# Kernel tuning notes

Hardware: AMD Instinct MI355X
Metric: run time of the kernel (lower is better)

## Reference

```python
import jax, jax.numpy as jnp
import numpy as np

D_MODEL = 1024
NUM_HEADS = 16
B, S = 2, 2048


def setup_inputs() -> dict:
    key = jax.random.key(0)
    ks = jax.random.split(key, 11)
    scale = 1.0 / np.sqrt(D_MODEL)
    inp = {
        'q': jax.random.normal(ks[0], (B, S, D_MODEL), jnp.float32),
        'k': jax.random.normal(ks[1], (B, S, D_MODEL), jnp.float32),
        'v': jax.random.normal(ks[2], (B, S, D_MODEL), jnp.float32),
        'w_q': jax.random.normal(ks[3], (D_MODEL, D_MODEL), jnp.float32) * scale,
        'b_q': jax.random.normal(ks[4], (D_MODEL,), jnp.float32) * 0.01,
        'w_k': jax.random.normal(ks[5], (D_MODEL, D_MODEL), jnp.float32) * scale,
        'b_k': jax.random.normal(ks[6], (D_MODEL,), jnp.float32) * 0.01,
        'w_v': jax.random.normal(ks[7], (D_MODEL, D_MODEL), jnp.float32) * scale,
        'b_v': jax.random.normal(ks[8], (D_MODEL,), jnp.float32) * 0.01,
        'w_o': jax.random.normal(ks[9], (D_MODEL, D_MODEL), jnp.float32) * scale,
        'b_o': jax.random.normal(ks[10], (D_MODEL,), jnp.float32) * 0.01,
    }
    return inp


def reference(q, k, v, w_q, b_q, w_k, b_k, w_v, b_v, w_o, b_o):
    Bq, Sq, D = q.shape
    H = NUM_HEADS
    dh = D // H
    # projections (weights stored as [in, out])
    query = q @ w_q + b_q
    key = k @ w_k + b_k
    value = v @ w_v + b_v
    # [B, S, D] -> [B, H, S, dh]
    query = query.reshape(Bq, Sq, H, dh).transpose(0, 2, 1, 3)
    key = key.reshape(Bq, -1, H, dh).transpose(0, 2, 1, 3)
    value = value.reshape(Bq, -1, H, dh).transpose(0, 2, 1, 3)
    # NOTE: original module does NOT scale by 1/sqrt(dh)
    scores = jnp.einsum('bhqd,bhkd->bhqk', query, key)  # [B,H,S,S]
    causal_mask = jnp.triu(jnp.ones((Sq, Sq), dtype=bool), k=1)  # True above diag
    scores = jnp.where(causal_mask[None, None], -jnp.inf, scores)
    attn = jax.nn.softmax(scores, axis=-1)
    data = jnp.einsum('bhqk,bhkd->bhqd', attn, value)  # [B,H,S,dh]
    # FAITHFUL to original bug: transpose(0,1) then view(B, S, -1)
    data = data.transpose(1, 0, 2, 3).reshape(Bq, Sq, -1)  # [H,B,S,dh] -> [B,S,D]
    return data @ w_o + b_o
```

## Files before the change

### kernel.cpp

```cpp
#include <hip/hip_runtime.h>

typedef __fp16 f16;
typedef __fp16 f16x8 __attribute__((ext_vector_type(8)));
typedef __fp16 f16x4 __attribute__((ext_vector_type(4)));
typedef __fp16 f16x2 __attribute__((ext_vector_type(2)));
typedef float f32x4 __attribute__((ext_vector_type(4)));
typedef float f32x16 __attribute__((ext_vector_type(16)));

#define D_MODEL 1024
#define SEQ 2048
#define NH 16
#define MTOT 4096

typedef const __attribute__((address_space(1))) unsigned int* gp1_t;
typedef __attribute__((address_space(3))) unsigned int* lp3_t;

__device__ __forceinline__ void gload_lds16(const void* g, void* l) {
  __builtin_amdgcn_global_load_lds((gp1_t)g, (lp3_t)l, 16, 0, 0);
}

__device__ __forceinline__ int permrow(int r) {
  int bp = r >> 11, u = (r >> 7) & 15, t = r & 127;
  int g16 = (bp << 4) | u;
  return ((((g16 & 1) << 4) | (g16 >> 1)) << 7) + t;
}

__device__ __forceinline__ unsigned int pkrtz(float a, float b) {
  union { f16x2 h; unsigned int u; } z;
  z.h = __builtin_amdgcn_cvt_pkrtz(a, b);
  return z.u;
}

__global__ __launch_bounds__(256) void cvt_all(const float* __restrict__ q,
                                               const float* __restrict__ k,
                                               const float* __restrict__ v,
                                               const float* __restrict__ wq,
                                               const float* __restrict__ wk,
                                               const float* __restrict__ wv,
                                               const float* __restrict__ wo,
                                               f16* __restrict__ qkv16,
                                               f16* __restrict__ wT) {
  __shared__ float tl[64][65];
  int bid = blockIdx.x, tid = threadIdx.x;
  if (bid < 6144) {
    int i = bid * 256 + tid;
    const int NT = (MTOT * D_MODEL) / 8;
    const float* src;
    int t;
    if (i < NT) { src = q; t = i; }
    else if (i < 2 * NT) { src = k; t = i - NT; }
    else { src = v; t = i - 2 * NT; }
    const float4* s4 = (const float4*)src;
    float4 a = s4[2 * t], b = s4[2 * t + 1];
    f16x8 h;
    h[0] = (f16)a.x; h[1] = (f16)a.y; h[2] = (f16)a.z; h[3] = (f16)a.w;
    h[4] = (f16)b.x; h[5] = (f16)b.y; h[6] = (f16)b.z; h[7] = (f16)b.w;
    *(f16x8*)(qkv16 + (size_t)i * 8) = h;
  } else {
    int bb = bid - 6144;
    int mat = bb >> 8, tile = bb & 255;
    int tk = (tile >> 4) << 6, tn = (tile & 15) << 6;
    const float* W = mat == 0 ? wq : mat == 1 ? wk : mat == 2 ? wv : wo;
    int rr = tid >> 4, c4 = (tid & 15) << 2;
#pragma unroll
    for (int it = 0; it < 4; ++it) {
      const float* p = W + (size_t)(tk + it * 16 + rr) * D_MODEL + tn + c4;
      float4 val = *(const float4*)p;
      tl[it * 16 + rr][c4 + 0] = val.x;
      tl[it * 16 + rr][c4 + 1] = val.y;
      tl[it * 16 + rr][c4 + 2] = val.z;
      tl[it * 16 + rr][c4 + 3] = val.w;
    }
    __syncthreads();
    int n = tid & 63, kseg = (tid >> 6) << 4;
    f16x8 lo, hi;
#pragma unroll
    for (int j = 0; j < 8; ++j) lo[j] = (f16)tl[kseg + j][n];
#pragma unroll
    for (int j = 0; j < 8; ++j) hi[j] = (f16)tl[kseg + 8 + j][n];
    f16* d = wT + (size_t)mat * (D_MODEL * D_MODEL) + (size_t)(tn + n) * D_MODEL + tk + kseg;
    *(f16x8*)d = lo;
    *(f16x8*)(d + 8) = hi;
  }
}

__global__ __launch_bounds__(256, 2) void gemm_qkv(const f16* __restrict__ q16,
                                                   const f16* __restrict__ k16,
                                                   const f16* __restrict__ v16,
                                                   const f16* __restrict__ wT,
                                                   const float* __restrict__ bq,
                                                   const float* __restrict__ bk,
                                                   const float* __restrict__ bv,
                                                   f16* __restrict__ Q16,
                                                   f16* __restrict__ K16,
                                                   f16* __restrict__ VT16) {
  const int K = D_MODEL, N = D_MODEL;
  const size_t WEL = (size_t)D_MODEL * D_MODEL;
  int z = blockIdx.z;
  const f16* A = z == 0 ? q16 : z == 1 ? k16 : v16;
  const f16* BT = wT + (size_t)z * WEL;
  const float* bias = z == 0 ? bq : z == 1 ? bk : bv;

  __shared__ f16 As[128 * 64];
  __shared__ f16 Bs[128 * 64];
  int tid = threadIdx.x;
  int w = tid >> 6, lane = tid & 63;
  int g = lane >> 4, c = lane & 15;
  int wr = w >> 1, wc = w & 1;
  int m0 = blockIdx.x * 128, n0 = blockIdx.y * 128;
  f32x4 acc[4][4] = {};

  for (int kt = 0; kt < K; kt += 64) {
#pragma unroll
    for (int i = 0; i < 4; ++i) {
      int seg = w * 4 + i;
      int p = seg * 1024 + lane * 16;
      int row = p >> 7;
      int colb = (p & 127) ^ ((row & 7) << 4);
      int ae = kt + (colb >> 1);
      gload_lds16(A + (size_t)(m0 + row) * K + ae, &As[seg * 512]);
      gload_lds16(BT + (size_t)(n0 + row) * K + ae, &Bs[seg * 512]);
    }
    __syncthreads();
    f16x8 af[4][2], bf[4][2];
#pragma unroll
    for (int m = 0; m < 4; ++m) {
#pragma unroll
      for (int kk = 0; kk < 2; ++kk) {
        int row = wr * 64 + m * 16 + c;
        int tb = (row * 128 + kk * 64 + g * 16) ^ ((row & 7) << 4);
        af[m][kk] = *(const f16x8*)((const char*)As + tb);
      }
    }
#pragma unroll
    for (int n = 0; n < 4; ++n) {
#pragma unroll
      for (int kk = 0; kk < 2; ++kk) {
        int row = wc * 64 + n * 16 + c;
        int tb = (row * 128 + kk * 64 + g * 16) ^ ((row & 7) << 4);
        bf[n][kk] = *(const f16x8*)((const char*)Bs + tb);
      }
    }
    __builtin_amdgcn_s_setprio(1);
#pragma unroll
    for (int m = 0; m < 4; ++m)
#pragma unroll
      for (int n = 0; n < 4; ++n)
#pragma unroll
        for (int kk = 0; kk < 2; ++kk)
          acc[m][n] = __builtin_amdgcn_mfma_f32_16x16x32_f16(af[m][kk], bf[n][kk], acc[m][n], 0, 0, 0);
    __builtin_amdgcn_s_setprio(0);
    __syncthreads();
  }

  int rb = m0 + wr * 64;
  int cb = n0 + wc * 64;
  if (z < 2) {
    f16* O = z == 0 ? Q16 : K16;
#pragma unroll
    for (int m = 0; m < 4; ++m) {
      int row0 = rb + m * 16 + 4 * g;
#pragma unroll
      for (int n = 0; n < 4; ++n) {
        int col = cb + n * 16 + c;
        float bv2 = bias[col];
#pragma unroll
        for (int r = 0; r < 4; ++r) O[(size_t)(row0 + r) * N + col] = (f16)(acc[m][n][r] + bv2);
      }
    }
  } else {
    f16* O = VT16;
#pragma unroll
    for (int m = 0; m < 4; ++m) {
      int s0f = rb + m * 16 + 4 * g;
      int bb = s0f >> 11, s = s0f & (SEQ - 1);
#pragma unroll
      for (int n = 0; n < 4; ++n) {
        int col = cb + n * 16 + c;
        float bv2 = bias[col];
        f16x4 hv;
#pragma unroll
        for (int r = 0; r < 4; ++r) hv[r] = (f16)(acc[m][n][r] + bv2);
        *(f16x4*)(O + ((size_t)(bb * NH + (col >> 6)) * 64 + (col & 63)) * SEQ + s) = hv;
      }
    }
  }
}

__global__ __launch_bounds__(256, 2) void gemm_out(const f16* __restrict__ A,
                                                   const f16* __restrict__ BT,
                                                   const float* __restrict__ bias,
                                                   float* __restrict__ O) {
  const int K = D_MODEL, N = D_MODEL;
  __shared__ f16 As[64 * 64];
  __shared__ f16 Bs[128 * 64];
  int tid = threadIdx.x;
  int w = tid >> 6, lane = tid & 63;
  int g = lane >> 4, c = lane & 15;
  int wr = w >> 1, wc = w & 1;
  int m0 = blockIdx.x * 64, n0 = blockIdx.y * 128;
  f32x4 acc[2][4] = {};

  for (int kt = 0; kt < K; kt += 64) {
#pragma unroll
    for (int i = 0; i < 2; ++i) {
      int seg = w * 2 + i;
      int p = seg * 1024 + lane * 16;
      int row = p >> 7;
      int colb = (p & 127) ^ ((row & 7) << 4);
      int ae = kt + (colb >> 1);
      gload_lds16(A + (size_t)permrow(m0 + row) * K + ae, &As[seg * 512]);
    }
#pragma unroll
    for (int i = 0; i < 4; ++i) {
      int seg = w * 4 + i;
      int p = seg * 1024 + lane * 16;
      int row = p >> 7;
      int colb = (p & 127) ^ ((row & 7) << 4);
      int ae = kt + (colb >> 1);
      gload_lds16(BT + (size_t)(n0 + row) * K + ae, &Bs[seg * 512]);
    }
    __syncthreads();
    f16x8 af[2][2], bf[4][2];
#pragma unroll
    for (int m = 0; m < 2; ++m) {
#pragma unroll
      for (int kk = 0; kk < 2; ++kk) {
        int row = wr * 32 + m * 16 + c;
        int tb = (row * 128 + kk * 64 + g * 16) ^ ((row & 7) << 4);
        af[m][kk] = *(const f16x8*)((const char*)As + tb);
      }
    }
#pragma unroll
    for (int n = 0; n < 4; ++n) {
#pragma unroll
      for (int kk = 0; kk < 2; ++kk) {
        int row = wc * 64 + n * 16 + c;
        int tb = (row * 128 + kk * 64 + g * 16) ^ ((row & 7) << 4);
        bf[n][kk] = *(const f16x8*)((const char*)Bs + tb);
      }
    }
    __builtin_amdgcn_s_setprio(1);
#pragma unroll
    for (int m = 0; m < 2; ++m)
#pragma unroll
      for (int n = 0; n < 4; ++n)
#pragma unroll
        for (int kk = 0; kk < 2; ++kk)
          acc[m][n] = __builtin_amdgcn_mfma_f32_16x16x32_f16(af[m][kk], bf[n][kk], acc[m][n], 0, 0, 0);
    __builtin_amdgcn_s_setprio(0);
    __syncthreads();
  }

  int rb = m0 + wr * 32;
  int cb = n0 + wc * 64;
#pragma unroll
  for (int m = 0; m < 2; ++m) {
    int row0 = rb + m * 16 + 4 * g;
#pragma unroll
    for (int n = 0; n < 4; ++n) {
      int col = cb + n * 16 + c;
      float bv = bias[col];
#pragma unroll
      for (int r = 0; r < 4; ++r) O[(size_t)(row0 + r) * N + col] = acc[m][n][r] + bv;
    }
  }
}

#define THR2 11.5f
__global__ __launch_bounds__(256, 2) void attn_kernel(const f16* __restrict__ Q,
                                                      const f16* __restrict__ K,
                                                      const f16* __restrict__ VT,
                                                      f16* __restrict__ AO) {
  __shared__ __attribute__((aligned(16))) f16 Ksh[2][2][64 * 64];
  __shared__ __attribute__((aligned(16))) f16 Vsh[2][2][64 * 64];
  const int BUFO = 2 * 64 * 64;
  int tid = threadIdx.x;
  int w = tid >> 6, lane = tid & 63;
  int c = lane & 31, hi = lane >> 5;
  int qh = w & 1, par = w >> 1;
  int blk = blockIdx.x;
  int bh = blk & 31;
  int uu = blk >> 5;
  int cb = 31 - uu;
  int b = bh >> 4, h = bh & 15;
  int q0 = cb * 64 + qh * 32;
  const int NT = cb + 1;
  const size_t brow = (size_t)b * SEQ;
  const int hcol = h * 64;

  int sr = lane >> 3;
  int seo = ((lane & 7) ^ sr) << 3;
  const f16* Kgb = K + (size_t)(brow + qh * 32 + sr) * D_MODEL + hcol + seo;
  const f16* Vgb = VT + ((size_t)bh * 64 + qh * 32 + sr) * SEQ + seo;
  f16* Kshf = &Ksh[0][0][0];
  f16* Vshf = &Vsh[0][0][0];
  f16* KshW = Kshf + par * 4096 + qh * 32 * 64;
  f16* VshW = Vshf + par * 4096 + qh * 32 * 64;

  const f16 LOG2E = (f16)1.44269504f;
  f16x8 qf[4];
  const f16* Qp = Q + (size_t)(brow + q0 + c) * D_MODEL + hcol + 8 * hi;
#pragma unroll
  for (int kk = 0; kk < 4; ++kk) {
    qf[kk] = *(const f16x8*)(Qp + 16 * kk);
#pragma unroll
    for (int j = 0; j < 8; ++j) qf[kk][j] = (f16)(qf[kk][j] * LOG2E);
  }

  float m_st = -1e30f, l_st = 0.f;
  f32x16 o0 = {}, o1 = {};

  if (par < NT) {
    int kv = par * 64;
#pragma unroll
    for (int j = 0; j < 4; ++j) {
      gload_lds16(Kgb + (size_t)(kv + j * 8) * D_MODEL, KshW + (j * 8) * 64);
      gload_lds16(Vgb + (size_t)(j * 8) * SEQ + kv, VshW + (j * 8) * 64);
    }
  }
  __syncthreads();

  int rsw = (c & 7) << 4;
  int cur = 0;
  const int U = (NT + 1) >> 1;
  for (int u = 0; u < U; ++u) {
    int tpre = 2 * u + 2 + par;
    if (tpre < NT) {
      int kv = tpre * 64;
      f16* kd = KshW + (cur ^ 1) * BUFO;
      f16* vd = VshW + (cur ^ 1) * BUFO;
#pragma unroll
      for (int j = 0; j < 4; ++j) {
        gload_lds16(Kgb + (size_t)(kv + j * 8) * D_MODEL, kd + (j * 8) * 64);
        gload_lds16(Vgb + (size_t)(j * 8) * SEQ + kv, vd + (j * 8) * 64);
      }
    }
    int t = 2 * u + par;
    if (t < NT) {
      const char* Kb = (const char*)(Kshf + cur * BUFO + par * 4096);
      const char* Vb = (const char*)(Vshf + cur * BUFO + par * 4096);
      f16x8 kf[2][4];
#pragma unroll
      for (int ks = 0; ks < 2; ++ks)
#pragma unroll
        for (int kk = 0; kk < 4; ++kk)
          kf[ks][kk] = *(const f16x8*)(Kb + (((ks * 32 + c) * 128 + 32 * kk + 16 * hi) ^ rsw));
      f32x16 s0 = {}, s1 = {};
      __builtin_amdgcn_s_setprio(1);
#pragma unroll
      for (int kk = 0; kk < 4; ++kk) {
        s0 = __builtin_amdgcn_mfma_f32_32x32x16_f16(kf[0][kk], qf[kk], s0, 0, 0, 0);
        s1 = __builtin_amdgcn_mfma_f32_32x32x16_f16(kf[1][kk], qf[kk], s1, 0, 0, 0);
      }
      __builtin_amdgcn_s_setprio(0);
      f16x8 vf[2][4];
#pragma unroll
      for (int dt = 0; dt < 2; ++dt)
#pragma unroll
        for (int kk = 0; kk < 4; ++kk)
          vf[dt][kk] = *(const f16x8*)(Vb + (((dt * 32 + c) * 128 + 32 * kk + 16 * hi) ^ rsw));
      if (t == NT - 1) {
        int q = q0 + c;
        int kvb = t * 64 + 4 * hi;
#pragma unroll
        for (int r = 0; r < 16; ++r) {
          int kv = kvb + (r & 3) + 8 * (r >> 2);
          if (kv > q) s0[r] = -1e30f;
          if (kv + 32 > q) s1[r] = -1e30f;
        }
      }
      float t8[8];
#pragma unroll
      for (int r = 0; r < 8; ++r)
        t8[r] = fmaxf(fmaxf(s0[r], s0[r + 8]), fmaxf(s1[r], s1[r + 8]));
      float pm = fmaxf(fmaxf(fmaxf(t8[0], t8[1]), fmaxf(t8[2], t8[3])),
                       fmaxf(fmaxf(t8[4], t8[5]), fmaxf(t8[6], t8[7])));
      float mx = fmaxf(pm, __shfl_xor(pm, 32));
      if (__any(mx > m_st + THR2)) {
        float mnew = fmaxf(m_st, mx);
        float corr = __builtin_amdgcn_exp2f(m_st - mnew);
        l_st *= corr;
#pragma unroll
        for (int r = 0; r < 16; ++r) { o0[r] *= corr; o1[r] *= corr; }
        m_st = mnew;
      }
      float ts[16];
#pragma unroll
      for (int r = 0; r < 16; ++r) {
        float p0 = __builtin_amdgcn_exp2f(s0[r] - m_st);
        float p1 = __builtin_amdgcn_exp2f(s1[r] - m_st);
        s0[r] = p0; s1[r] = p1;
        ts[r] = p0 + p1;
      }
#pragma unroll
      for (int st = 8; st > 0; st >>= 1)
#pragma unroll
        for (int r = 0; r < st; ++r) ts[r] += ts[r + st];
      l_st += ts[0];
      union PU { unsigned int u[4]; f16x8 v; };
      PU pu[4];
#pragma unroll
      for (int kk = 0; kk < 4; ++kk) {
        int rb = 8 * (kk & 1);
        unsigned int la0, la1, lb0, lb1;
        if (kk < 2) {
          la0 = pkrtz(s0[rb + 0], s0[rb + 1]);
          la1 = pkrtz(s0[rb + 2], s0[rb + 3]);
          lb0 = pkrtz(s0[rb + 4], s0[rb + 5]);
          lb1 = pkrtz(s0[rb + 6], s0[rb + 7]);
        } else {
          la0 = pkrtz(s1[rb + 0], s1[rb + 1]);
          la1 = pkrtz(s1[rb + 2], s1[rb + 3]);
          lb0 = pkrtz(s1[rb + 4], s1[rb + 5]);
          lb1 = pkrtz(s1[rb + 6], s1[rb + 7]);
        }
        asm("v_permlane32_swap_b32 %0, %1" : "+v"(la0), "+v"(lb0));
        asm("v_permlane32_swap_b32 %0, %1" : "+v"(la1), "+v"(lb1));
        pu[kk].u[0] = la0; pu[kk].u[1] = la1; pu[kk].u[2] = lb0; pu[kk].u[3] = lb1;
      }
      __builtin_amdgcn_s_setprio(1);
#pragma unroll
      for (int kk = 0; kk < 4; ++kk) {
        o0 = __builtin_amdgcn_mfma_f32_32x32x16_f16(vf[0][kk], pu[kk].v, o0, 0, 0, 0);
        o1 = __builtin_amdgcn_mfma_f32_32x32x16_f16(vf[1][kk], pu[kk].v, o1, 0, 0, 0);
      }
      __builtin_amdgcn_s_setprio(0);
    }
    __syncthreads();
    cur ^= 1;
  }

  float* sc = (float*)Kshf;
  int mb = (qh * 64 + lane) * 34;
  if (par == 1) {
    sc[mb] = m_st;
    sc[mb + 1] = l_st;
#pragma unroll
    for (int r = 0; r < 16; ++r) { sc[mb + 2 + r] = o0[r]; sc[mb + 18 + r] = o1[r]; }
  }
  __syncthreads();
  if (par == 0) {
    float m1 = sc[mb], l1 = sc[mb + 1];
    float mm = fmaxf(m_st, m1);
    float c0 = __builtin_amdgcn_exp2f(m_st - mm);
    float c1 = __builtin_amdgcn_exp2f(m1 - mm);
    float l = l_st * c0 + l1 * c1;
#pragma unroll
    for (int r = 0; r < 16; ++r) {
      o0[r] = o0[r] * c0 + sc[mb + 2 + r] * c1;
      o1[r] = o1[r] * c0 + sc[mb + 18 + r] * c1;
    }
    float lt = l + __shfl_xor(l, 32);
    float linv = 1.0f / lt;
    f16* aoq = AO + ((size_t)bh * SEQ + q0 + c) * 64 + 4 * hi;
#pragma unroll
    for (int rq = 0; rq < 4; ++rq) {
      f16x4 h0, h1;
#pragma unroll
      for (int r = 0; r < 4; ++r) {
        h0[r] = (f16)(o0[4 * rq + r] * linv);
        h1[r] = (f16)(o1[4 * rq + r] * linv);
      }
      *(f16x4*)(aoq + 8 * rq) = h0;
      *(f16x4*)(aoq + 32 + 8 * rq) = h1;
    }
  }
}

extern "C" void kernel_launch(void* const* d_in, const int* in_sizes, int n_in,
                              void* d_out, int out_size, void* d_ws, size_t ws_size,
                              hipStream_t stream) {
  const float* q  = (const float*)d_in[0];
  const float* k  = (const float*)d_in[1];
  const float* v  = (const float*)d_in[2];
  const float* wq = (const float*)d_in[3];
  const float* bq = (const float*)d_in[4];
  const float* wk = (const float*)d_in[5];
  const float* bk = (const float*)d_in[6];
  const float* wv = (const float*)d_in[7];
  const float* bv = (const float*)d_in[8];
  const float* wo = (const float*)d_in[9];
  const float* bo = (const float*)d_in[10];

  const size_t TEN = (size_t)MTOT * D_MODEL;
  const size_t WEL = (size_t)D_MODEL * D_MODEL;
  f16* ws  = (f16*)d_ws;
  f16* q16 = ws;
  f16* k16 = q16 + TEN;
  f16* v16 = k16 + TEN;
  f16* wT  = v16 + TEN;
  f16* Q16 = wT + 4 * WEL;
  f16* K16 = Q16 + TEN;
  f16* VT16 = K16 + TEN;
  f16* AO  = q16;

  cvt_all<<<7168, 256, 0, stream>>>(q, k, v, wq, wk, wv, wo, q16, wT);
  gemm_qkv<<<dim3(32, 8, 3), 256, 0, stream>>>(q16, k16, v16, wT, bq, bk, bv, Q16, K16, VT16);
  attn_kernel<<<1024, 256, 0, stream>>>(Q16, K16, VT16, AO);
  gemm_out<<<dim3(64, 8), 256, 0, stream>>>(AO, wT + 3 * WEL, bo, (float*)d_out);
}
```

Before: 110.8 us.

## Restructure QKV GEMM to 256x256 tiles with double-buffered LDS prefetch

```diff
diff --git a/kernel.cpp b/kernel.cpp
--- a/kernel.cpp
+++ b/kernel.cpp
@@ -84,7 +84,8 @@
   }
 }
 
-__global__ __launch_bounds__(256, 2) void gemm_qkv(const f16* __restrict__ q16,
+#define QTILE (256 * 64)
+__global__ __launch_bounds__(512, 2) void gemm_qkv(const f16* __restrict__ q16,
                                                    const f16* __restrict__ k16,
                                                    const f16* __restrict__ v16,
                                                    const f16* __restrict__ wT,
@@ -94,6 +95,7 @@
                                                    f16* __restrict__ Q16,
                                                    f16* __restrict__ K16,
                                                    f16* __restrict__ VT16) {
+  extern __shared__ __attribute__((aligned(16))) f16 sm[];
   const int K = D_MODEL, N = D_MODEL;
   const size_t WEL = (size_t)D_MODEL * D_MODEL;
   int z = blockIdx.z;
@@ -101,64 +103,140 @@
   const f16* BT = wT + (size_t)z * WEL;
   const float* bias = z == 0 ? bq : z == 1 ? bk : bv;
 
-  __shared__ f16 As[128 * 64];
-  __shared__ f16 Bs[128 * 64];
   int tid = threadIdx.x;
   int w = tid >> 6, lane = tid & 63;
   int g = lane >> 4, c = lane & 15;
-  int wr = w >> 1, wc = w & 1;
-  int m0 = blockIdx.x * 128, n0 = blockIdx.y * 128;
-  f32x4 acc[4][4] = {};
-
-  for (int kt = 0; kt < K; kt += 64) {
-#pragma unroll
-    for (int i = 0; i < 4; ++i) {
-      int seg = w * 4 + i;
-      int p = seg * 1024 + lane * 16;
-      int row = p >> 7;
-      int colb = (p & 127) ^ ((row & 7) << 4);
-      int ae = kt + (colb >> 1);
-      gload_lds16(A + (size_t)(m0 + row) * K + ae, &As[seg * 512]);
-      gload_lds16(BT + (size_t)(n0 + row) * K + ae, &Bs[seg * 512]);
-    }
-    __syncthreads();
-    f16x8 af[4][2], bf[4][2];
-#pragma unroll
-    for (int m = 0; m < 4; ++m) {
-#pragma unroll
-      for (int kk = 0; kk < 2; ++kk) {
-        int row = wr * 64 + m * 16 + c;
-        int tb = (row * 128 + kk * 64 + g * 16) ^ ((row & 7) << 4);
-        af[m][kk] = *(const f16x8*)((const char*)As + tb);
-      }
-    }
-#pragma unroll
-    for (int n = 0; n < 4; ++n) {
-#pragma unroll
-      for (int kk = 0; kk < 2; ++kk) {
-        int row = wc * 64 + n * 16 + c;
-        int tb = (row * 128 + kk * 64 + g * 16) ^ ((row & 7) << 4);
-        bf[n][kk] = *(const f16x8*)((const char*)Bs + tb);
-      }
-    }
+  int wr = w >> 2, wc = w & 3;
+  int m0 = blockIdx.x * 256, n0 = blockIdx.y * 256;
+  f32x4 acc[8][4] = {};
+
+  int sr = lane >> 3;
+  int sc8 = ((lane & 7) ^ sr) << 3;
+  const f16* Ag = A + (size_t)(m0 + w * 32 + sr) * K + sc8;
+  const f16* Bg = BT + (size_t)(n0 + w * 32 + sr) * K + sc8;
+
+  {
+    f16* A0 = sm;
+    f16* B0 = sm + QTILE;
+#pragma unroll
+    for (int j = 0; j < 4; ++j) {
+      gload_lds16(Ag + (size_t)(j * 8) * K, A0 + (w * 32 + j * 8) * 64);
+      gload_lds16(Bg + (size_t)(j * 8) * K, B0 + (w * 32 + j * 8) * 64);
+    }
+  }
+  __syncthreads();
+
+  const int NKT = K / 64;
+  for (int t = 0; t < NKT; ++t) {
+    const char* Ac = (const char*)(sm + (t & 1) * 2 * QTILE);
+    const char* Bc = Ac + QTILE * 2;
+    f16* An = sm + ((t + 1) & 1) * 2 * QTILE;
+    f16* Bn = An + QTILE;
+    const f16* Agt = Ag + (t + 1) * 64;
+    const f16* Bgt = Bg + (t + 1) * 64;
+    bool pre = (t + 1 < NKT);
+
+    f16x8 af[4][2], bf[2][2];
+#pragma unroll
+    for (int mi = 0; mi < 4; ++mi)
+#pragma unroll
+      for (int kk = 0; kk < 2; ++kk) {
+        int row = wr * 128 + mi * 16 + c;
+        af[mi][kk] = *(const f16x8*)(Ac + ((row * 128 + kk * 64 + g * 16) ^ ((row & 7) << 4)));
+      }
+#pragma unroll
+    for (int ni = 0; ni < 2; ++ni)
+#pragma unroll
+      for (int kk = 0; kk < 2; ++kk) {
+        int row = wc * 64 + ni * 16 + c;
+        bf[ni][kk] = *(const f16x8*)(Bc + ((row * 128 + kk * 64 + g * 16) ^ ((row & 7) << 4)));
+      }
+    if (pre) {
+      gload_lds16(Agt, An + (w * 32) * 64);
+      gload_lds16(Agt + (size_t)(8) * K, An + (w * 32 + 8) * 64);
+    }
+    __builtin_amdgcn_s_barrier();
     __builtin_amdgcn_s_setprio(1);
 #pragma unroll
-    for (int m = 0; m < 4; ++m)
-#pragma unroll
-      for (int n = 0; n < 4; ++n)
+    for (int mi = 0; mi < 4; ++mi)
+#pragma unroll
+      for (int ni = 0; ni < 2; ++ni)
 #pragma unroll
         for (int kk = 0; kk < 2; ++kk)
-          acc[m][n] = __builtin_amdgcn_mfma_f32_16x16x32_f16(af[m][kk], bf[n][kk], acc[m][n], 0, 0, 0);
+          acc[mi][ni] = __builtin_amdgcn_mfma_f32_16x16x32_f16(af[mi][kk], bf[ni][kk], acc[mi][ni], 0, 0, 0);
+    __builtin_amdgcn_s_setprio(0);
+#pragma unroll
+    for (int ni = 0; ni < 2; ++ni)
+#pragma unroll
+      for (int kk = 0; kk < 2; ++kk) {
+        int row = wc * 64 + (2 + ni) * 16 + c;
+        bf[ni][kk] = *(const f16x8*)(Bc + ((row * 128 + kk * 64 + g * 16) ^ ((row & 7) << 4)));
+      }
+    if (pre) {
+      gload_lds16(Agt + (size_t)(16) * K, An + (w * 32 + 16) * 64);
+      gload_lds16(Agt + (size_t)(24) * K, An + (w * 32 + 24) * 64);
+    }
+    __builtin_amdgcn_s_barrier();
+    __builtin_amdgcn_s_setprio(1);
+#pragma unroll
+    for (int mi = 0; mi < 4; ++mi)
+#pragma unroll
+      for (int ni = 0; ni < 2; ++ni)
+#pragma unroll
+        for (int kk = 0; kk < 2; ++kk)
+          acc[mi][2 + ni] = __builtin_amdgcn_mfma_f32_16x16x32_f16(af[mi][kk], bf[ni][kk], acc[mi][2 + ni], 0, 0, 0);
+    __builtin_amdgcn_s_setprio(0);
+#pragma unroll
+    for (int mi = 0; mi < 4; ++mi)
+#pragma unroll
+      for (int kk = 0; kk < 2; ++kk) {
+        int row = wr * 128 + 64 + mi * 16 + c;
+        af[mi][kk] = *(const f16x8*)(Ac + ((row * 128 + kk * 64 + g * 16) ^ ((row & 7) << 4)));
+      }
+    if (pre) {
+      gload_lds16(Bgt, Bn + (w * 32) * 64);
+      gload_lds16(Bgt + (size_t)(8) * K, Bn + (w * 32 + 8) * 64);
+    }
+    __builtin_amdgcn_s_barrier();
+    __builtin_amdgcn_s_setprio(1);
+#pragma unroll
+    for (int mi = 0; mi < 4; ++mi)
+#pragma unroll
+      for (int ni = 0; ni < 2; ++ni)
+#pragma unroll
+        for (int kk = 0; kk < 2; ++kk)
+          acc[4 + mi][2 + ni] = __builtin_amdgcn_mfma_f32_16x16x32_f16(af[mi][kk], bf[ni][kk], acc[4 + mi][2 + ni], 0, 0, 0);
+    __builtin_amdgcn_s_setprio(0);
+#pragma unroll
+    for (int ni = 0; ni < 2; ++ni)
+#pragma unroll
+      for (int kk = 0; kk < 2; ++kk) {
+        int row = wc * 64 + ni * 16 + c;
+        bf[ni][kk] = *(const f16x8*)(Bc + ((row * 128 + kk * 64 + g * 16) ^ ((row & 7) << 4)));
+      }
+    if (pre) {
+      gload_lds16(Bgt + (size_t)(16) * K, Bn + (w * 32 + 16) * 64);
+      gload_lds16(Bgt + (size_t)(24) * K, Bn + (w * 32 + 24) * 64);
+    }
+    __builtin_amdgcn_s_barrier();
+    __builtin_amdgcn_s_setprio(1);
+#pragma unroll
+    for (int mi = 0; mi < 4; ++mi)
+#pragma unroll
+      for (int ni = 0; ni < 2; ++ni)
+#pragma unroll
+        for (int kk = 0; kk < 2; ++kk)
+          acc[4 + mi][ni] = __builtin_amdgcn_mfma_f32_16x16x32_f16(af[mi][kk], bf[ni][kk], acc[4 + mi][ni], 0, 0, 0);
     __builtin_amdgcn_s_setprio(0);
     __syncthreads();
   }
 
-  int rb = m0 + wr * 64;
+  int rb = m0 + wr * 128;
   int cb = n0 + wc * 64;
   if (z < 2) {
     f16* O = z == 0 ? Q16 : K16;
 #pragma unroll
-    for (int m = 0; m < 4; ++m) {
+    for (int m = 0; m < 8; ++m) {
       int row0 = rb + m * 16 + 4 * g;
 #pragma unroll
       for (int n = 0; n < 4; ++n) {
@@ -171,7 +249,7 @@
   } else {
     f16* O = VT16;
 #pragma unroll
-    for (int m = 0; m < 4; ++m) {
+    for (int m = 0; m < 8; ++m) {
       int s0f = rb + m * 16 + 4 * g;
       int bb = s0f >> 11, s = s0f & (SEQ - 1);
 #pragma unroll
@@ -495,8 +573,15 @@
   f16* VT16 = K16 + TEN;
   f16* AO  = q16;
 
+  static bool attr_set = false;
+  if (!attr_set) {
+    hipFuncSetAttribute(reinterpret_cast<const void*>(&gemm_qkv),
+                        hipFuncAttributeMaxDynamicSharedMemorySize, 131072);
+    attr_set = true;
+  }
+
   cvt_all<<<7168, 256, 0, stream>>>(q, k, v, wq, wk, wv, wo, q16, wT);
-  gemm_qkv<<<dim3(32, 8, 3), 256, 0, stream>>>(q16, k16, v16, wT, bq, bk, bv, Q16, K16, VT16);
+  gemm_qkv<<<dim3(16, 4, 3), 512, 131072, stream>>>(q16, k16, v16, wT, bq, bk, bv, Q16, K16, VT16);
   attn_kernel<<<1024, 256, 0, stream>>>(Q16, K16, VT16, AO);
   gemm_out<<<dim3(64, 8), 256, 0, stream>>>(AO, wT + 3 * WEL, bo, (float*)d_out);
 }
```

After: 107.3 us. 3.1% less time.

## Restructure QKV GEMM into 256x256 tiles with 4-stage async LDS pipeline

Applied to the files above, without the earlier changes.

```diff
diff --git a/kernel.cpp b/kernel.cpp
--- a/kernel.cpp
+++ b/kernel.cpp
@@ -84,7 +84,8 @@
   }
 }
 
-__global__ __launch_bounds__(256, 2) void gemm_qkv(const f16* __restrict__ q16,
+#define SLOT_ELEM 16384
+__global__ __launch_bounds__(512, 2) void gemm_qkv(const f16* __restrict__ q16,
                                                    const f16* __restrict__ k16,
                                                    const f16* __restrict__ v16,
                                                    const f16* __restrict__ wT,
@@ -94,6 +95,7 @@
                                                    f16* __restrict__ Q16,
                                                    f16* __restrict__ K16,
                                                    f16* __restrict__ VT16) {
+  extern __shared__ __attribute__((aligned(16))) f16 sm[];
   const int K = D_MODEL, N = D_MODEL;
   const size_t WEL = (size_t)D_MODEL * D_MODEL;
   int z = blockIdx.z;
@@ -101,64 +103,77 @@
   const f16* BT = wT + (size_t)z * WEL;
   const float* bias = z == 0 ? bq : z == 1 ? bk : bv;
 
-  __shared__ f16 As[128 * 64];
-  __shared__ f16 Bs[128 * 64];
   int tid = threadIdx.x;
   int w = tid >> 6, lane = tid & 63;
   int g = lane >> 4, c = lane & 15;
-  int wr = w >> 1, wc = w & 1;
-  int m0 = blockIdx.x * 128, n0 = blockIdx.y * 128;
-  f32x4 acc[4][4] = {};
-
-  for (int kt = 0; kt < K; kt += 64) {
-#pragma unroll
-    for (int i = 0; i < 4; ++i) {
-      int seg = w * 4 + i;
-      int p = seg * 1024 + lane * 16;
-      int row = p >> 7;
-      int colb = (p & 127) ^ ((row & 7) << 4);
-      int ae = kt + (colb >> 1);
-      gload_lds16(A + (size_t)(m0 + row) * K + ae, &As[seg * 512]);
-      gload_lds16(BT + (size_t)(n0 + row) * K + ae, &Bs[seg * 512]);
-    }
-    __syncthreads();
-    f16x8 af[4][2], bf[4][2];
-#pragma unroll
-    for (int m = 0; m < 4; ++m) {
-#pragma unroll
-      for (int kk = 0; kk < 2; ++kk) {
-        int row = wr * 64 + m * 16 + c;
-        int tb = (row * 128 + kk * 64 + g * 16) ^ ((row & 7) << 4);
-        af[m][kk] = *(const f16x8*)((const char*)As + tb);
-      }
-    }
-#pragma unroll
-    for (int n = 0; n < 4; ++n) {
-#pragma unroll
-      for (int kk = 0; kk < 2; ++kk) {
-        int row = wc * 64 + n * 16 + c;
-        int tb = (row * 128 + kk * 64 + g * 16) ^ ((row & 7) << 4);
-        bf[n][kk] = *(const f16x8*)((const char*)Bs + tb);
-      }
-    }
+  int wr = w >> 2, wc = w & 3;
+  int m0 = blockIdx.x * 256, n0 = blockIdx.y * 256;
+  f32x4 acc[8][4] = {};
+
+  int sl0 = lane >> 3, s = lane & 7;
+  int u = s ^ sl0;
+  int rlow = u >> 2, gsl = u & 3;
+  const f16* Agp = A + (size_t)(m0 + w * 32 + 2 * sl0 + rlow) * K + gsl * 8;
+  const f16* Bgp = BT + (size_t)(n0 + w * 32 + 2 * sl0 + rlow) * K + gsl * 8;
+
+#define STAGE_QKV(tt, bi)                                                    \
+  {                                                                          \
+    f16* dA = sm + (bi)*SLOT_ELEM + w * 1024;                                \
+    f16* dB = dA + 8192;                                                     \
+    const f16* sa = Agp + (size_t)(tt)*32;                                   \
+    const f16* sb = Bgp + (size_t)(tt)*32;                                   \
+    gload_lds16(sa, dA);                                                     \
+    gload_lds16(sa + (size_t)16 * K, dA + 512);                              \
+    gload_lds16(sb, dB);                                                     \
+    gload_lds16(sb + (size_t)16 * K, dB + 512);                              \
+  }
+
+  STAGE_QKV(0, 0)
+  STAGE_QKV(1, 1)
+  STAGE_QKV(2, 2)
+
+  const int NKT = K / 32;
+  for (int t = 0; t < NKT; ++t) {
+    if (t < NKT - 2) asm volatile("s_waitcnt vmcnt(8)" ::: "memory");
+    else if (t == NKT - 2) asm volatile("s_waitcnt vmcnt(4)" ::: "memory");
+    else asm volatile("s_waitcnt vmcnt(0)" ::: "memory");
+    __builtin_amdgcn_sched_barrier(0);
+    __builtin_amdgcn_s_barrier();
+    __builtin_amdgcn_sched_barrier(0);
+    if (t + 3 < NKT) STAGE_QKV(t + 3, (t + 3) & 3)
+
+    const char* Ac = (const char*)(sm + (t & 3) * SLOT_ELEM);
+    const char* Bc = Ac + 16384;
+    f16x8 af[8], bf[4];
+#pragma unroll
+    for (int mi = 0; mi < 8; ++mi) {
+      int row = wr * 128 + mi * 16 + c;
+      int tb = (row >> 1) * 128 + (((((row & 1) << 2) | g) ^ ((row >> 1) & 7)) << 4);
+      af[mi] = *(const f16x8*)(Ac + tb);
+    }
+#pragma unroll
+    for (int ni = 0; ni < 4; ++ni) {
+      int row = wc * 64 + ni * 16 + c;
+      int tb = (row >> 1) * 128 + (((((row & 1) << 2) | g) ^ ((row >> 1) & 7)) << 4);
+      bf[ni] = *(const f16x8*)(Bc + tb);
+    }
+    asm volatile("s_waitcnt lgkmcnt(0)" ::: "memory");
+    __builtin_amdgcn_sched_barrier(0);
     __builtin_amdgcn_s_setprio(1);
 #pragma unroll
-    for (int m = 0; m < 4; ++m)
-#pragma unroll
-      for (int n = 0; n < 4; ++n)
-#pragma unroll
-        for (int kk = 0; kk < 2; ++kk)
-          acc[m][n] = __builtin_amdgcn_mfma_f32_16x16x32_f16(af[m][kk], bf[n][kk], acc[m][n], 0, 0, 0);
+    for (int mi = 0; mi < 8; ++mi)
+#pragma unroll
+      for (int ni = 0; ni < 4; ++ni)
+        acc[mi][ni] = __builtin_amdgcn_mfma_f32_16x16x32_f16(af[mi], bf[ni], acc[mi][ni], 0, 0, 0);
     __builtin_amdgcn_s_setprio(0);
-    __syncthreads();
-  }
-
-  int rb = m0 + wr * 64;
+  }
+
+  int rb = m0 + wr * 128;
   int cb = n0 + wc * 64;
   if (z < 2) {
     f16* O = z == 0 ? Q16 : K16;
 #pragma unroll
-    for (int m = 0; m < 4; ++m) {
+    for (int m = 0; m < 8; ++m) {
       int row0 = rb + m * 16 + 4 * g;
 #pragma unroll
       for (int n = 0; n < 4; ++n) {
@@ -171,9 +186,9 @@
   } else {
     f16* O = VT16;
 #pragma unroll
-    for (int m = 0; m < 4; ++m) {
+    for (int m = 0; m < 8; ++m) {
       int s0f = rb + m * 16 + 4 * g;
-      int bb = s0f >> 11, s = s0f & (SEQ - 1);
+      int bb = s0f >> 11, ss = s0f & (SEQ - 1);
 #pragma unroll
       for (int n = 0; n < 4; ++n) {
         int col = cb + n * 16 + c;
@@ -181,7 +196,7 @@
         f16x4 hv;
 #pragma unroll
         for (int r = 0; r < 4; ++r) hv[r] = (f16)(acc[m][n][r] + bv2);
-        *(f16x4*)(O + ((size_t)(bb * NH + (col >> 6)) * 64 + (col & 63)) * SEQ + s) = hv;
+        *(f16x4*)(O + ((size_t)(bb * NH + (col >> 6)) * 64 + (col & 63)) * SEQ + ss) = hv;
       }
     }
   }
@@ -495,8 +510,15 @@
   f16* VT16 = K16 + TEN;
   f16* AO  = q16;
 
+  static bool attr_set = false;
+  if (!attr_set) {
+    hipFuncSetAttribute(reinterpret_cast<const void*>(&gemm_qkv),
+                        hipFuncAttributeMaxDynamicSharedMemorySize, 131072);
+    attr_set = true;
+  }
+
   cvt_all<<<7168, 256, 0, stream>>>(q, k, v, wq, wk, wv, wo, q16, wT);
-  gemm_qkv<<<dim3(32, 8, 3), 256, 0, stream>>>(q16, k16, v16, wT, bq, bk, bv, Q16, K16, VT16);
+  gemm_qkv<<<dim3(16, 4, 3), 512, 131072, stream>>>(q16, k16, v16, wT, bq, bk, bv, Q16, K16, VT16);
   attn_kernel<<<1024, 256, 0, stream>>>(Q16, K16, VT16, AO);
   gemm_out<<<dim3(64, 8), 256, 0, stream>>>(AO, wT + 3 * WEL, bo, (float*)d_out);
 }
```

Result: no change. 109.2 us (-1.4%).

## Fuse fp32-to-fp16 input conversion into double-buffered QKV projection GEMM

Applied to the files above, without the earlier changes.

```diff
diff --git a/kernel.cpp b/kernel.cpp
--- a/kernel.cpp
+++ b/kernel.cpp
@@ -31,62 +31,41 @@
   return z.u;
 }
 
-__global__ __launch_bounds__(256) void cvt_all(const float* __restrict__ q,
-                                               const float* __restrict__ k,
-                                               const float* __restrict__ v,
-                                               const float* __restrict__ wq,
+__global__ __launch_bounds__(256) void cvt_all(const float* __restrict__ wq,
                                                const float* __restrict__ wk,
                                                const float* __restrict__ wv,
                                                const float* __restrict__ wo,
-                                               f16* __restrict__ qkv16,
                                                f16* __restrict__ wT) {
   __shared__ float tl[64][65];
-  int bid = blockIdx.x, tid = threadIdx.x;
-  if (bid < 6144) {
-    int i = bid * 256 + tid;
-    const int NT = (MTOT * D_MODEL) / 8;
-    const float* src;
-    int t;
-    if (i < NT) { src = q; t = i; }
-    else if (i < 2 * NT) { src = k; t = i - NT; }
-    else { src = v; t = i - 2 * NT; }
-    const float4* s4 = (const float4*)src;
-    float4 a = s4[2 * t], b = s4[2 * t + 1];
-    f16x8 h;
-    h[0] = (f16)a.x; h[1] = (f16)a.y; h[2] = (f16)a.z; h[3] = (f16)a.w;
-    h[4] = (f16)b.x; h[5] = (f16)b.y; h[6] = (f16)b.z; h[7] = (f16)b.w;
-    *(f16x8*)(qkv16 + (size_t)i * 8) = h;
-  } else {
-    int bb = bid - 6144;
-    int mat = bb >> 8, tile = bb & 255;
-    int tk = (tile >> 4) << 6, tn = (tile & 15) << 6;
-    const float* W = mat == 0 ? wq : mat == 1 ? wk : mat == 2 ? wv : wo;
-    int rr = tid >> 4, c4 = (tid & 15) << 2;
-#pragma unroll
-    for (int it = 0; it < 4; ++it) {
-      const float* p = W + (size_t)(tk + it * 16 + rr) * D_MODEL + tn + c4;
-      float4 val = *(const float4*)p;
-      tl[it * 16 + rr][c4 + 0] = val.x;
-      tl[it * 16 + rr][c4 + 1] = val.y;
-      tl[it * 16 + rr][c4 + 2] = val.z;
-      tl[it * 16 + rr][c4 + 3] = val.w;
-    }
-    __syncthreads();
-    int n = tid & 63, kseg = (tid >> 6) << 4;
-    f16x8 lo, hi;
-#pragma unroll
-    for (int j = 0; j < 8; ++j) lo[j] = (f16)tl[kseg + j][n];
-#pragma unroll
-    for (int j = 0; j < 8; ++j) hi[j] = (f16)tl[kseg + 8 + j][n];
-    f16* d = wT + (size_t)mat * (D_MODEL * D_MODEL) + (size_t)(tn + n) * D_MODEL + tk + kseg;
-    *(f16x8*)d = lo;
-    *(f16x8*)(d + 8) = hi;
-  }
-}
-
-__global__ __launch_bounds__(256, 2) void gemm_qkv(const f16* __restrict__ q16,
-                                                   const f16* __restrict__ k16,
-                                                   const f16* __restrict__ v16,
+  int bb = blockIdx.x, tid = threadIdx.x;
+  int mat = bb >> 8, tile = bb & 255;
+  int tk = (tile >> 4) << 6, tn = (tile & 15) << 6;
+  const float* W = mat == 0 ? wq : mat == 1 ? wk : mat == 2 ? wv : wo;
+  int rr = tid >> 4, c4 = (tid & 15) << 2;
+#pragma unroll
+  for (int it = 0; it < 4; ++it) {
+    const float* p = W + (size_t)(tk + it * 16 + rr) * D_MODEL + tn + c4;
+    float4 val = *(const float4*)p;
+    tl[it * 16 + rr][c4 + 0] = val.x;
+    tl[it * 16 + rr][c4 + 1] = val.y;
+    tl[it * 16 + rr][c4 + 2] = val.z;
+    tl[it * 16 + rr][c4 + 3] = val.w;
+  }
+  __syncthreads();
+  int n = tid & 63, kseg = (tid >> 6) << 4;
+  f16x8 lo, hi;
+#pragma unroll
+  for (int j = 0; j < 8; ++j) lo[j] = (f16)tl[kseg + j][n];
+#pragma unroll
+  for (int j = 0; j < 8; ++j) hi[j] = (f16)tl[kseg + 8 + j][n];
+  f16* d = wT + (size_t)mat * (D_MODEL * D_MODEL) + (size_t)(tn + n) * D_MODEL + tk + kseg;
+  *(f16x8*)d = lo;
+  *(f16x8*)(d + 8) = hi;
+}
+
+__global__ __launch_bounds__(256, 2) void gemm_qkv(const float* __restrict__ q32,
+                                                   const float* __restrict__ k32,
+                                                   const float* __restrict__ v32,
                                                    const f16* __restrict__ wT,
                                                    const float* __restrict__ bq,
                                                    const float* __restrict__ bk,
@@ -94,15 +73,15 @@
                                                    f16* __restrict__ Q16,
                                                    f16* __restrict__ K16,
                                                    f16* __restrict__ VT16) {
+  __shared__ __attribute__((aligned(16))) f16 As[2][128 * 64];
+  __shared__ __attribute__((aligned(16))) f16 Bs[2][128 * 64];
   const int K = D_MODEL, N = D_MODEL;
   const size_t WEL = (size_t)D_MODEL * D_MODEL;
   int z = blockIdx.z;
-  const f16* A = z == 0 ? q16 : z == 1 ? k16 : v16;
+  const float* A32 = z == 0 ? q32 : z == 1 ? k32 : v32;
   const f16* BT = wT + (size_t)z * WEL;
   const float* bias = z == 0 ? bq : z == 1 ? bk : bv;
 
-  __shared__ f16 As[128 * 64];
-  __shared__ f16 Bs[128 * 64];
   int tid = threadIdx.x;
   int w = tid >> 6, lane = tid & 63;
   int g = lane >> 4, c = lane & 15;
@@ -110,37 +89,77 @@
   int m0 = blockIdx.x * 128, n0 = blockIdx.y * 128;
   f32x4 acc[4][4] = {};
 
+  int arow = tid >> 1, ah = tid & 1;
+  const float* Ag = A32 + (size_t)(m0 + arow) * K + ah * 32;
+  char* AwBase0 = (char*)&As[0][0];
+  char* AwBase1 = (char*)&As[1][0];
+  int awoff[4];
+#pragma unroll
+  for (int u = 0; u < 4; ++u)
+    awoff[u] = (arow * 128 + ah * 64 + u * 16) ^ ((arow & 7) << 4);
+
+#define STAGE_B(kt, bi)                                                       \
+  {                                                                           \
+    _Pragma("unroll") for (int i = 0; i < 4; ++i) {                           \
+      int seg = w * 4 + i;                                                    \
+      int p = seg * 1024 + lane * 16;                                         \
+      int row = p >> 7;                                                       \
+      int colb = (p & 127) ^ ((row & 7) << 4);                                \
+      int ae = (kt) + (colb >> 1);                                            \
+      gload_lds16(BT + (size_t)(n0 + row) * K + ae, &Bs[bi][seg * 512]);      \
+    }                                                                         \
+  }
+
+#define LOAD_A(kt)                                                            \
+  {                                                                           \
+    const float4* a4 = (const float4*)(Ag + (kt));                            \
+    _Pragma("unroll") for (int j = 0; j < 8; ++j) av[j] = a4[j];              \
+  }
+
+#define WRITE_A(base)                                                         \
+  {                                                                           \
+    _Pragma("unroll") for (int u = 0; u < 4; ++u) {                           \
+      union { unsigned int uu[4]; f16x8 v; } pw;                              \
+      pw.uu[0] = pkrtz(av[2 * u].x, av[2 * u].y);                             \
+      pw.uu[1] = pkrtz(av[2 * u].z, av[2 * u].w);                             \
+      pw.uu[2] = pkrtz(av[2 * u + 1].x, av[2 * u + 1].y);                     \
+      pw.uu[3] = pkrtz(av[2 * u + 1].z, av[2 * u + 1].w);                     \
+      *(f16x8*)((base) + awoff[u]) = pw.v;                                    \
+    }                                                                         \
+  }
+
+  float4 av[8];
+  LOAD_A(0)
+  STAGE_B(0, 0)
+  WRITE_A(AwBase0)
+  __syncthreads();
+
   for (int kt = 0; kt < K; kt += 64) {
-#pragma unroll
-    for (int i = 0; i < 4; ++i) {
-      int seg = w * 4 + i;
-      int p = seg * 1024 + lane * 16;
-      int row = p >> 7;
-      int colb = (p & 127) ^ ((row & 7) << 4);
-      int ae = kt + (colb >> 1);
-      gload_lds16(A + (size_t)(m0 + row) * K + ae, &As[seg * 512]);
-      gload_lds16(BT + (size_t)(n0 + row) * K + ae, &Bs[seg * 512]);
-    }
-    __syncthreads();
+    int cur = (kt >> 6) & 1, nxt = cur ^ 1;
+    bool pre = (kt + 64) < K;
+    if (pre) {
+      LOAD_A(kt + 64)
+      STAGE_B(kt + 64, nxt)
+    }
+    const char* Ac = (const char*)&As[cur][0];
+    const char* Bc = (const char*)&Bs[cur][0];
     f16x8 af[4][2], bf[4][2];
 #pragma unroll
-    for (int m = 0; m < 4; ++m) {
+    for (int m = 0; m < 4; ++m)
 #pragma unroll
       for (int kk = 0; kk < 2; ++kk) {
         int row = wr * 64 + m * 16 + c;
         int tb = (row * 128 + kk * 64 + g * 16) ^ ((row & 7) << 4);
-        af[m][kk] = *(const f16x8*)((const char*)As + tb);
-      }
-    }
-#pragma unroll
-    for (int n = 0; n < 4; ++n) {
+        af[m][kk] = *(const f16x8*)(Ac + tb);
+      }
+#pragma unroll
+    for (int n = 0; n < 4; ++n)
 #pragma unroll
       for (int kk = 0; kk < 2; ++kk) {
         int row = wc * 64 + n * 16 + c;
         int tb = (row * 128 + kk * 64 + g * 16) ^ ((row & 7) << 4);
-        bf[n][kk] = *(const f16x8*)((const char*)Bs + tb);
-      }
-    }
+        bf[n][kk] = *(const f16x8*)(Bc + tb);
+      }
     __builtin_amdgcn_s_setprio(1);
 #pragma unroll
     for (int m = 0; m < 4; ++m)
@@ -150,6 +169,7 @@
         for (int kk = 0; kk < 2; ++kk)
           acc[m][n] = __builtin_amdgcn_mfma_f32_16x16x32_f16(af[m][kk], bf[n][kk], acc[m][n], 0, 0, 0);
     __builtin_amdgcn_s_setprio(0);
+    if (pre) WRITE_A(nxt ? AwBase1 : AwBase0)
     __syncthreads();
   }
 
@@ -173,7 +193,7 @@
 #pragma unroll
     for (int m = 0; m < 4; ++m) {
       int s0f = rb + m * 16 + 4 * g;
-      int bb = s0f >> 11, s = s0f & (SEQ - 1);
+      int bb = s0f >> 11, ss = s0f & (SEQ - 1);
 #pragma unroll
       for (int n = 0; n < 4; ++n) {
         int col = cb + n * 16 + c;
@@ -181,7 +201,7 @@
         f16x4 hv;
 #pragma unroll
         for (int r = 0; r < 4; ++r) hv[r] = (f16)(acc[m][n][r] + bv2);
-        *(f16x4*)(O + ((size_t)(bb * NH + (col >> 6)) * 64 + (col & 63)) * SEQ + s) = hv;
+        *(f16x4*)(O + ((size_t)(bb * NH + (col >> 6)) * 64 + (col & 63)) * SEQ + ss) = hv;
       }
     }
   }
@@ -487,16 +507,14 @@
   const size_t WEL = (size_t)D_MODEL * D_MODEL;
   f16* ws  = (f16*)d_ws;
   f16* q16 = ws;
-  f16* k16 = q16 + TEN;
-  f16* v16 = k16 + TEN;
-  f16* wT  = v16 + TEN;
+  f16* wT  = q16 + 3 * TEN;
   f16* Q16 = wT + 4 * WEL;
   f16* K16 = Q16 + TEN;
   f16* VT16 = K16 + TEN;
   f16* AO  = q16;
 
-  cvt_all<<<7168, 256, 0, stream>>>(q, k, v, wq, wk, wv, wo, q16, wT);
-  gemm_qkv<<<dim3(32, 8, 3), 256, 0, stream>>>(q16, k16, v16, wT, bq, bk, bv, Q16, K16, VT16);
+  cvt_all<<<1024, 256, 0, stream>>>(wq, wk, wv, wo, wT);
+  gemm_qkv<<<dim3(32, 8, 3), 256, 0, stream>>>(q, k, v, wT, bq, bk, bv, Q16, K16, VT16);
   attn_kernel<<<1024, 256, 0, stream>>>(Q16, K16, VT16, AO);
   gemm_out<<<dim3(64, 8), 256, 0, stream>>>(AO, wT + 3 * WEL, bo, (float*)d_out);
 }
```

Result: slower. 134.9 us (+21.8%).
